# Kernel optimization log

Measured on AMD Instinct MI355X. Metric: run time of the kernel, lower is better.

Reference implementation:

```python
import jax, jax.numpy as jnp
import numpy as np

EMBEDDING_DIM = 1024


def setup_inputs() -> dict:
    key = jax.random.key(0)
    x = jax.random.normal(key, (8, 4096, EMBEDDING_DIM), dtype=jnp.float32)
    return {"x": x}


def reference(x):
    # x: [B, S, D]. pe[pos, i] = sin(pos / 10000**((i//2)/S)) if i even else cos(...)
    # NOTE: faithful to source: exponent denominator is len_sequence S, not D.
    S = x.shape[1]
    D = x.shape[2]
    pos = jnp.arange(S, dtype=jnp.float32)[:, None]            # [S, 1]
    i = jnp.arange(D)                                          # [D]
    k = (i // 2).astype(jnp.float32)[None, :]                  # [1, D]
    angle = pos / jnp.power(jnp.float32(10000.0), k / jnp.float32(S))  # [S, D]
    pe = jnp.where((i % 2 == 0)[None, :], jnp.sin(angle), jnp.cos(angle))
    return x + pe[None, :, :].astype(x.dtype)
```

## Files before the change

kernel.cpp:

```cpp
#include <hip/hip_runtime.h>


#define PE_S    4096
#define PE_D    1024
#define N4      (8 * PE_S * PE_D / 4)
#define BLOCKS  2048
#define THREADS 256
#define STRIDE  (BLOCKS * THREADS)
#define ITERS   (N4 / STRIDE)

typedef float f32x4 __attribute__((ext_vector_type(4)));

__global__ __launch_bounds__(THREADS, 8) void PositionalEncoding_84095459656362_kernel(
    const float* __restrict__ x, float* __restrict__ out) {
    const int i0 = blockIdx.x * THREADS + threadIdx.x;
    const int d4 = (i0 & (PE_D / 4 - 1)) << 2;
    const int s0 = i0 >> 8;

    const float c  = -0.0032440703857f;
    const float r1 = 0.99775390625f;
    const float e0 = __builtin_exp2f((float)(d4 >> 1) * c);

    const float ae0 = (float)s0 * e0;
    const float ae1 = ae0 * r1;
    const float ao0 = (float)(s0 + 2048) * e0;
    const float ao1 = ao0 * r1;

    float sa, ca, sb, cb;
    f32x4 pe0, pe1;
    __sincosf(ae0, &sa, &ca);
    __sincosf(ae1, &sb, &cb);
    pe0.x = sa; pe0.y = ca; pe0.z = sb; pe0.w = cb;
    __sincosf(ao0, &sa, &ca);
    __sincosf(ao1, &sb, &cb);
    pe1.x = sa; pe1.y = ca; pe1.z = sb; pe1.w = cb;

    const f32x4* xin = (const f32x4*)x + i0;
    f32x4*       o   = (f32x4*)out     + i0;

    f32x4 v0 = xin[0];
    f32x4 v1 = xin[STRIDE];
#pragma unroll
    for (int k = 0; k < ITERS - 2; k += 2) {
        const f32x4 n0 = xin[(k + 2) * STRIDE];
        const f32x4 n1 = xin[(k + 3) * STRIDE];
        o[k * STRIDE]       = v0 + pe0;
        o[(k + 1) * STRIDE] = v1 + pe1;
        v0 = n0;
        v1 = n1;
    }
    o[(ITERS - 2) * STRIDE] = v0 + pe0;
    o[(ITERS - 1) * STRIDE] = v1 + pe1;
}

extern "C" void kernel_launch(void* const* d_in, const int* in_sizes, int n_in,
                              void* d_out, int out_size, void* d_ws, size_t ws_size,
                              hipStream_t stream) {
    const float* x = (const float*)d_in[0];
    float* out = (float*)d_out;
    PositionalEncoding_84095459656362_kernel<<<BLOCKS, THREADS, 0, stream>>>(x, out);
}
```

Measured before the change: 244.1 us.

## Switch to contiguous per-block chunks and compute sincos per row

```diff
diff --git a/kernel.cpp b/kernel.cpp
--- a/kernel.cpp
+++ b/kernel.cpp
@@ -4,53 +4,48 @@
 #define PE_S    4096
 #define PE_D    1024
 #define N4      (8 * PE_S * PE_D / 4)
-#define BLOCKS  2048
 #define THREADS 256
-#define STRIDE  (BLOCKS * THREADS)
-#define ITERS   (N4 / STRIDE)
+#define ITERS   16
+#define CHUNK   (THREADS * ITERS)
+#define BLOCKS  (N4 / CHUNK)
 
 typedef float f32x4 __attribute__((ext_vector_type(4)));
 
+__device__ __forceinline__ f32x4 pe_vec(float a0, float r1) {
+    float sa, ca, sb, cb;
+    __sincosf(a0, &sa, &ca);
+    __sincosf(a0 * r1, &sb, &cb);
+    f32x4 p; p.x = sa; p.y = ca; p.z = sb; p.w = cb;
+    return p;
+}
+
 __global__ __launch_bounds__(THREADS, 8) void PositionalEncoding_84095459656362_kernel(
     const float* __restrict__ x, float* __restrict__ out) {
-    const int i0 = blockIdx.x * THREADS + threadIdx.x;
-    const int d4 = (i0 & (PE_D / 4 - 1)) << 2;
-    const int s0 = i0 >> 8;
+    const int tid   = threadIdx.x;
+    const int base  = blockIdx.x * CHUNK + tid;
+    const int d4    = tid << 2;
+    const int sBase = (base >> 8) & (PE_S - 1);
 
     const float c  = -0.0032440703857f;
     const float r1 = 0.99775390625f;
     const float e0 = __builtin_exp2f((float)(d4 >> 1) * c);
 
-    const float ae0 = (float)s0 * e0;
-    const float ae1 = ae0 * r1;
-    const float ao0 = (float)(s0 + 2048) * e0;
-    const float ao1 = ao0 * r1;
+    const f32x4* xin = (const f32x4*)x + base;
+    f32x4*       o   = (f32x4*)out     + base;
 
-    float sa, ca, sb, cb;
-    f32x4 pe0, pe1;
-    __sincosf(ae0, &sa, &ca);
-    __sincosf(ae1, &sb, &cb);
-    pe0.x = sa; pe0.y = ca; pe0.z = sb; pe0.w = cb;
-    __sincosf(ao0, &sa, &ca);
-    __sincosf(ao1, &sb, &cb);
-    pe1.x = sa; pe1.y = ca; pe1.z = sb; pe1.w = cb;
-
-    const f32x4* xin = (const f32x4*)x + i0;
-    f32x4*       o   = (f32x4*)out     + i0;
-
-    f32x4 v0 = xin[0];
-    f32x4 v1 = xin[STRIDE];
+    f32x4 v0 = xin[0 * THREADS];
+    f32x4 v1 = xin[1 * THREADS];
 #pragma unroll
     for (int k = 0; k < ITERS - 2; k += 2) {
-        const f32x4 n0 = xin[(k + 2) * STRIDE];
-        const f32x4 n1 = xin[(k + 3) * STRIDE];
-        o[k * STRIDE]       = v0 + pe0;
-        o[(k + 1) * STRIDE] = v1 + pe1;
+        const f32x4 n0 = xin[(k + 2) * THREADS];
+        const f32x4 n1 = xin[(k + 3) * THREADS];
+        o[k * THREADS]       = v0 + pe_vec((float)(sBase + k)     * e0, r1);
+        o[(k + 1) * THREADS] = v1 + pe_vec((float)(sBase + k + 1) * e0, r1);
         v0 = n0;
         v1 = n1;
     }
-    o[(ITERS - 2) * STRIDE] = v0 + pe0;
-    o[(ITERS - 1) * STRIDE] = v1 + pe1;
+    o[(ITERS - 2) * THREADS] = v0 + pe_vec((float)(sBase + ITERS - 2) * e0, r1);
+    o[(ITERS - 1) * THREADS] = v1 + pe_vec((float)(sBase + ITERS - 1) * e0, r1);
 }
 
 extern "C" void kernel_launch(void* const* d_in, const int* in_sizes, int n_in,
```

New measurement: 232.9 us. 1.05x faster.
